# Performance work log

Measured on AMD Instinct MI355X. Metric: run time of the kernel, lower is better.

The kernel has to match this reference:

```python
import jax, jax.numpy as jnp
import numpy as np

B, T, V, E, H = 32, 128, 32000, 512, 1024
START = 1


def setup_inputs() -> dict:
    key = jax.random.key(0)
    ks = jax.random.split(key, 16)
    s = 0.02
    inp = {
        'h0': jax.random.normal(ks[0], (B, H), jnp.float32),
        'c0': jax.random.normal(ks[1], (B, H), jnp.float32),
        'h1': jax.random.normal(ks[2], (B, H), jnp.float32),
        'c1': jax.random.normal(ks[3], (B, H), jnp.float32),
        'h2': jax.random.normal(ks[4], (B, H), jnp.float32),
        'c2': jax.random.normal(ks[5], (B, H), jnp.float32),
        'h3': jax.random.normal(ks[6], (B, H), jnp.float32),
        'c3': jax.random.normal(ks[7], (B, H), jnp.float32),
        'emb': jax.random.normal(ks[8], (V, E), jnp.float32) * s,
        'Wx0': jax.random.normal(ks[9], (E, 4 * H), jnp.float32) * s,
        'Wh0': jax.random.normal(ks[10], (H, 4 * H), jnp.float32) * s,
        'b0': jnp.zeros((4 * H,), jnp.float32),
        'Wx1': jax.random.normal(ks[11], (H, 4 * H), jnp.float32) * s,
        'Wh1': jax.random.normal(ks[12], (H, 4 * H), jnp.float32) * s,
        'b1': jnp.zeros((4 * H,), jnp.float32),
        'Wx2': jax.random.normal(ks[13], (H, 4 * H), jnp.float32) * s,
        'Wh2': jax.random.normal(ks[14], (H, 4 * H), jnp.float32) * s,
        'b2': jnp.zeros((4 * H,), jnp.float32),
        'Wx3': jax.random.normal(ks[15], (H, 4 * H), jnp.float32) * s,
        'Wh3': jax.random.normal(jax.random.fold_in(key, 99), (H, 4 * H), jnp.float32) * s,
        'b3': jnp.zeros((4 * H,), jnp.float32),
        'fcW': jax.random.normal(jax.random.fold_in(key, 100), (H, V), jnp.float32) * s,
        'fcb': jnp.zeros((V,), jnp.float32),
        'target_length': T,
    }
    return inp


def _lstm_cell(x, h, c, Wx, Wh, b):
    # Keras gate order: i, f, c(candidate), o
    z = x @ Wx + h @ Wh + b  # [B, 4H]
    i, f, g, o = jnp.split(z, 4, axis=-1)
    i = jax.nn.sigmoid(i)
    f = jax.nn.sigmoid(f)
    g = jnp.tanh(g)
    o = jax.nn.sigmoid(o)
    c_new = f * c + i * g
    h_new = o * jnp.tanh(c_new)
    return h_new, c_new


def reference(h0, c0, h1, c1, h2, c2, h3, c3, emb,
              Wx0, Wh0, b0, Wx1, Wh1, b1, Wx2, Wh2, b2, Wx3, Wh3, b3,
              fcW, fcb, target_length):
    n_batch = h0.shape[0]
    tok0 = jnp.full((n_batch,), START, dtype=jnp.int32)

    def step(carry, _):
        tok, h0, c0, h1, c1, h2, c2, h3, c3 = carry
        x = emb[tok]  # [B, E]
        h0, c0 = _lstm_cell(x, h0, c0, Wx0, Wh0, b0)
        h1, c1 = _lstm_cell(h0, h1, c1, Wx1, Wh1, b1)
        h2, c2 = _lstm_cell(h1, h2, c2, Wx2, Wh2, b2)
        h3, c3 = _lstm_cell(h2, h3, c3, Wx3, Wh3, b3)
        logits = h3 @ fcW + fcb  # [B, V]
        tok = jnp.argmax(logits, axis=1).astype(jnp.int32)
        return (tok, h0, c0, h1, c1, h2, c2, h3, c3), (logits, tok)

    carry0 = (tok0, h0, c0, h1, c1, h2, c2, h3, c3)
    _, (logits_seq, ids_seq) = jax.lax.scan(step, carry0, None, length=target_length)
    outputs_prob = jnp.transpose(logits_seq, (1, 0, 2))  # [B, T, V]
    outputs = jnp.transpose(ids_seq, (1, 0))             # [B, T]
    return outputs_prob, outputs
```

## Files before the change

kernel.cpp:

```cpp
#include <hip/hip_runtime.h>
#include <stdint.h>

#define NBLK 256
#define NTHR 512

typedef _Float16 f16;
typedef _Float16 f16x8 __attribute__((ext_vector_type(8)));
typedef float f32x4 __attribute__((ext_vector_type(4)));
typedef unsigned long long u64;


__device__ __forceinline__ void split2(float w, f16& hi, f16& lo) {
  f16 h = (__builtin_fabsf(w) < 6.104e-05f) ? (f16)0.0f : (f16)w;
  hi = h;
  lo = (f16)((w - (float)h) * 2048.0f);
}

__device__ __forceinline__ void split3(float w, f16& h, f16& l, f16& m) {
  const float hf = (__builtin_fabsf(w) < 6.104e-05f) ? 0.0f : (float)(f16)w;
  h = (f16)hf;
  const float r1s = (w - hf) * 2048.0f;
  const float lf = (__builtin_fabsf(r1s) < 6.104e-05f) ? 0.0f : (float)(f16)r1s;
  l = (f16)lf;
  const float r2s = (r1s - lf) * 2048.0f;
  m = (__builtin_fabsf(r2s) < 6.104e-05f) ? (f16)0.0f : (f16)r2s;
}

__device__ __forceinline__ float sig32(float z) {
  const float e32 = (float)exp(-(double)z);
  return 1.0f / __fadd_rn(1.0f, e32);
}
__device__ __forceinline__ float tanh32f(float z) { return (float)tanh((double)z); }

__device__ __forceinline__ u64 packvc(float v, unsigned col) {
  unsigned u = __float_as_uint(v);
  u = (u & 0x80000000u) ? ~u : (u | 0x80000000u);
  return ((u64)u << 32) | (u64)(0xFFFFFFFFu - col);
}
__device__ __forceinline__ u64 umax64(u64 a, u64 b) { return a > b ? a : b; }


struct MainP {
  const float* emb;
  const float* bias[4];
  const float* fcb;
  const float* hini[4];
  const float* cini[4];
  const f16* Whi[4];
  const f16* Wlo[4];
  const f16* fchi;
  const f16* fclo;
  f16* axh[5];
  f16* axl[5];
  f16* axm[5];
  u64* top;
  unsigned* bar;
  float* out;
};

struct PrepP {
  const float* src[9];
  f16* dhi[9];
  f16* dlo[9];
  int srcK[9];
  int srcN[9];
  int dstK[9];
  int koff[9];
  int base[9];
  unsigned* bar;
};


__device__ __forceinline__ void grid_barrier(unsigned* cnt, unsigned* gen) {
  __syncthreads();
  if (threadIdx.x == 0) {
    unsigned g = __hip_atomic_load(gen, __ATOMIC_RELAXED, __HIP_MEMORY_SCOPE_AGENT);
    unsigned prev = __hip_atomic_fetch_add(cnt, 1u, __ATOMIC_ACQ_REL, __HIP_MEMORY_SCOPE_AGENT);
    if (prev == (unsigned)(NBLK - 1)) {
      __hip_atomic_store(cnt, 0u, __ATOMIC_RELAXED, __HIP_MEMORY_SCOPE_AGENT);
      __hip_atomic_store(gen, g + 1u, __ATOMIC_RELEASE, __HIP_MEMORY_SCOPE_AGENT);
    } else {
      while (__hip_atomic_load(gen, __ATOMIC_RELAXED, __HIP_MEMORY_SCOPE_AGENT) == g) {
        __builtin_amdgcn_s_sleep(1);
      }
      __builtin_amdgcn_fence(__ATOMIC_ACQUIRE, "agent");
    }
  }
  __syncthreads();
}


__global__ __launch_bounds__(256) void prep_split(PrepP p) {
  const int bid = blockIdx.x;
  const int tid = threadIdx.x;
  if (bid == 0 && tid == 0) { p.bar[0] = 0; p.bar[1] = 0; }

  int job = 0;
#pragma unroll
  for (int j2 = 1; j2 < 9; ++j2) job += (bid >= p.base[j2]) ? 1 : 0;
  const int tile = bid - p.base[job];
  const float* src = p.src[job];
  f16* dhi = p.dhi[job];
  f16* dlo = p.dlo[job];
  const int srcN = p.srcN[job];
  const int dstK = p.dstK[job];
  const int koff = p.koff[job];
  const int nK = p.srcK[job] >> 6;
  const int tk = tile % nK;
  const int tc = tile / nK;

  __shared__ float lds[64][65];
  {
    const int j = tid & 63, i0 = tid >> 6;
#pragma unroll
    for (int r = 0; r < 16; ++r) {
      const int i = r * 4 + i0;
      lds[i][j] = src[(size_t)(tk * 64 + i) * srcN + tc * 64 + j];
    }
  }
  __syncthreads();
  {
    const int jc = tid >> 2, part = tid & 3;
    f16x8 h0v, l0v, h1v, l1v;
#pragma unroll
    for (int ii = 0; ii < 8; ++ii) {
      f16 a, b;
      split2(lds[part * 16 + ii][jc], a, b);
      h0v[ii] = a; l0v[ii] = b;
    }
#pragma unroll
    for (int ii = 0; ii < 8; ++ii) {
      f16 a, b;
      split2(lds[part * 16 + 8 + ii][jc], a, b);
      h1v[ii] = a; l1v[ii] = b;
    }
    const size_t db = (size_t)(tc * 64 + jc) * dstK + koff + tk * 64 + part * 16;
    *(f16x8*)(dhi + db) = h0v;
    *(f16x8*)(dhi + db + 8) = h1v;
    *(f16x8*)(dlo + db) = l0v;
    *(f16x8*)(dlo + db + 8) = l1v;
  }
}

__global__ void ws_sentinel(float* out) {
  if (blockIdx.x == 0 && threadIdx.x == 0) out[0] = 1.0e9f;
}


__global__ __launch_bounds__(NTHR, 2) void lstm_main(MainP p) {
  const int blk = blockIdx.x;
  const int tid = threadIdx.x;
  const int lane = tid & 63;
  const int w = tid >> 6;
  const int q = lane >> 4;
  const int n16 = lane & 15;

  __shared__ float zpart[8][2][32][16];
  __shared__ float fcpart[2][32][128];
  __shared__ float zred[32][16];
  __shared__ float cst[4][32][4];
  __shared__ f16 hs_h[32][4];
  __shared__ f16 hs_l[32][4];
  __shared__ f16 hs_m[32][4];
  __shared__ int tokS[32];
  __shared__ u64 redu[32][16];

  unsigned* bcnt = p.bar;
  unsigned* bgen = p.bar + 1;

  for (int i = tid; i < 512; i += NTHR) {
    const int l = i >> 7, b = (i >> 2) & 31, j = i & 3;
    cst[l][b][j] = p.cini[l][b * 1024 + 4 * blk + j];
    f16 hh, ll, mm;
    split3(p.hini[l][b * 1024 + 4 * blk + j], hh, ll, mm);
    if (l == 0) {
      p.axh[0][b * 1024 + 4 * blk + j] = hh;
      p.axl[0][b * 1024 + 4 * blk + j] = ll;
      p.axm[0][b * 1024 + 4 * blk + j] = mm;
    } else {
      p.axh[l][b * 2048 + 1024 + 4 * blk + j] = hh;
      p.axl[l][b * 2048 + 1024 + 4 * blk + j] = ll;
      p.axm[l][b * 2048 + 1024 + 4 * blk + j] = mm;
    }
  }
  grid_barrier(bcnt, bgen);

  const int col16 = 1024 * (n16 >> 2) + 4 * blk + (n16 & 3);

  auto layer_tail = [&](int l, const float* bias, f16* dh, f16* dl, f16* dm, int dstride) {
    __syncthreads();
    {
      const int row = tid >> 4, c = tid & 15;
      double A = 0.0, B = 0.0;
#pragma unroll
      for (int w2 = 0; w2 < 8; ++w2) {
        A += (double)zpart[w2][0][row][c];
        B += (double)zpart[w2][1][row][c];
      }
      zred[row][c] = __fadd_rn(__fadd_rn((float)A, (float)B),
                               bias[1024 * (c >> 2) + 4 * blk + (c & 3)]);
    }
    __syncthreads();
    if (tid < 128) {
      const int b = tid >> 2, j = tid & 3;
      const float zi = zred[b][j], zf = zred[b][4 + j], zg = zred[b][8 + j], zo = zred[b][12 + j];
      const float i_ = sig32(zi);
      const float f_ = sig32(zf);
      const float g_ = tanh32f(zg);
      const float o_ = sig32(zo);
      const float c_ = __fadd_rn(__fmul_rn(f_, cst[l][b][j]), __fmul_rn(i_, g_));
      cst[l][b][j] = c_;
      const float h_ = __fmul_rn(o_, tanh32f(c_));
      f16 hh, ll, mm;
      split3(h_, hh, ll, mm);
      hs_h[b][j] = hh; hs_l[b][j] = ll; hs_m[b][j] = mm;
      dh[b * dstride + 4 * blk + j] = hh;
      dl[b * dstride + 4 * blk + j] = ll;
      dm[b * dstride + 4 * blk + j] = mm;
    }
  };

  for (int t = 0; t < 128; ++t) {
    if (t == 0) {
      if (tid < 32) tokS[tid] = 1;
    } else {
      const int row = tid >> 4, seg = tid & 15;
      const u64* tr = p.top + row * 256 + seg * 16;
      u64 m = 0;
#pragma unroll
      for (int e = 0; e < 16; ++e) m = umax64(m, tr[e]);
      redu[row][seg] = m;
      __syncthreads();
      if (tid < 32) {
        u64 mm = redu[tid][0];
#pragma unroll
        for (int s2 = 1; s2 < 16; ++s2) mm = umax64(mm, redu[tid][s2]);
        const int tok = (int)(0xFFFFFFFFu - (unsigned)(mm & 0xFFFFFFFFull));
        tokS[tid] = tok;
        if (blk == tid)
          p.out[(size_t)32 * 128 * 32000 + (size_t)tid * 128 + (t - 1)] = (float)tok;
      }
    }
    __syncthreads();

    {
      double zdA0[4] = {0,0,0,0}, zdA1[4] = {0,0,0,0};
      double zdB0[4] = {0,0,0,0}, zdB1[4] = {0,0,0,0};
      const size_t wrow = (size_t)col16 * 1536;
      const f32x4 zz = {0.f, 0.f, 0.f, 0.f};
#pragma unroll
      for (int sl = 0; sl < 6; ++sl) {
        const int k0 = (w * 6 + sl) * 32 + 8 * q;
        const f16x8 bh = *(const f16x8*)(p.Whi[0] + wrow + k0);
        const f16x8 bl = *(const f16x8*)(p.Wlo[0] + wrow + k0);
        f16x8 ah0, al0, am0, ah1, al1, am1;
        if (k0 < 512) {
          {
            const float* ep = p.emb + (size_t)tokS[n16] * 512 + k0;
            const float4 v0 = *(const float4*)ep;
            const float4 v1 = *(const float4*)(ep + 4);
            const float vv[8] = {v0.x, v0.y, v0.z, v0.w, v1.x, v1.y, v1.z, v1.w};
#pragma unroll
            for (int e = 0; e < 8; ++e) { f16 a,b,c; split3(vv[e],a,b,c); ah0[e]=a; al0[e]=b; am0[e]=c; }
          }
          {
            const float* ep = p.emb + (size_t)tokS[16 + n16] * 512 + k0;
            const float4 v0 = *(const float4*)ep;
            const float4 v1 = *(const float4*)(ep + 4);
            const float vv[8] = {v0.x, v0.y, v0.z, v0.w, v1.x, v1.y, v1.z, v1.w};
#pragma unroll
            for (int e = 0; e < 8; ++e) { f16 a,b,c; split3(vv[e],a,b,c); ah1[e]=a; al1[e]=b; am1[e]=c; }
          }
        } else {
          const int ks = k0 - 512;
          ah0 = *(const f16x8*)(p.axh[0] + n16 * 1024 + ks);
          al0 = *(const f16x8*)(p.axl[0] + n16 * 1024 + ks);
          am0 = *(const f16x8*)(p.axm[0] + n16 * 1024 + ks);
          ah1 = *(const f16x8*)(p.axh[0] + (16 + n16) * 1024 + ks);
          al1 = *(const f16x8*)(p.axl[0] + (16 + n16) * 1024 + ks);
          am1 = *(const f16x8*)(p.axm[0] + (16 + n16) * 1024 + ks);
        }
        f32x4 t00 = __builtin_amdgcn_mfma_f32_16x16x32_f16(ah0, bh, zz, 0, 0, 0);
        f32x4 t10 = __builtin_amdgcn_mfma_f32_16x16x32_f16(ah0, bl, zz, 0, 0, 0);
        t10 = __builtin_amdgcn_mfma_f32_16x16x32_f16(al0, bh, t10, 0, 0, 0);
        f32x4 t20 = __builtin_amdgcn_mfma_f32_16x16x32_f16(al0, bl, zz, 0, 0, 0);
        t20 = __builtin_amdgcn_mfma_f32_16x16x32_f16(am0, bh, t20, 0, 0, 0);
        f32x4 t01 = __builtin_amdgcn_mfma_f32_16x16x32_f16(ah1, bh, zz, 0, 0, 0);
        f32x4 t11 = __builtin_amdgcn_mfma_f32_16x16x32_f16(ah1, bl, zz, 0, 0, 0);
        t11 = __builtin_amdgcn_mfma_f32_16x16x32_f16(al1, bh, t11, 0, 0, 0);
        f32x4 t21 = __builtin_amdgcn_mfma_f32_16x16x32_f16(al1, bl, zz, 0, 0, 0);
        t21 = __builtin_amdgcn_mfma_f32_16x16x32_f16(am1, bh, t21, 0, 0, 0);
        if (k0 < 512) {
#pragma unroll
          for (int r = 0; r < 4; ++r) {
            zdA0[r] += (double)t00[r] + (double)t10[r] * 0x1p-11 + (double)t20[r] * 0x1p-22;
            zdA1[r] += (double)t01[r] + (double)t11[r] * 0x1p-11 + (double)t21[r] * 0x1p-22;
          }
        } else {
#pragma unroll
          for (int r = 0; r < 4; ++r) {
            zdB0[r] += (double)t00[r] + (double)t10[r] * 0x1p-11 + (double)t20[r] * 0x1p-22;
            zdB1[r] += (double)t01[r] + (double)t11[r] * 0x1p-11 + (double)t21[r] * 0x1p-22;
          }
        }
      }
#pragma unroll
      for (int r = 0; r < 4; ++r) {
        zpart[w][0][4 * q + r][n16] = (float)zdA0[r];
        zpart[w][0][16 + 4 * q + r][n16] = (float)zdA1[r];
        zpart[w][1][4 * q + r][n16] = (float)zdB0[r];
        zpart[w][1][16 + 4 * q + r][n16] = (float)zdB1[r];
      }
    }
    layer_tail(0, p.bias[0], p.axh[1], p.axl[1], p.axm[1], 2048);
    grid_barrier(bcnt, bgen);

    for (int l = 1; l < 4; ++l) {
      if (tid < 128) {
        const int b = tid >> 2, j = tid & 3;
        if (l == 1) {
          p.axh[0][b * 1024 + 4 * blk + j] = hs_h[b][j];
          p.axl[0][b * 1024 + 4 * blk + j] = hs_l[b][j];
          p.axm[0][b * 1024 + 4 * blk + j] = hs_m[b][j];
        } else {
          p.axh[l - 1][b * 2048 + 1024 + 4 * blk + j] = hs_h[b][j];
          p.axl[l - 1][b * 2048 + 1024 + 4 * blk + j] = hs_l[b][j];
          p.axm[l - 1][b * 2048 + 1024 + 4 * blk + j] = hs_m[b][j];
        }
      }
      {
        double zdA0[4] = {0,0,0,0}, zdA1[4] = {0,0,0,0};
        double zdB0[4] = {0,0,0,0}, zdB1[4] = {0,0,0,0};
        const f16* Whi_ = p.Whi[l];
        const f16* Wlo_ = p.Wlo[l];
        const f16* axh_ = p.axh[l];
        const f16* axl_ = p.axl[l];
        const f16* axm_ = p.axm[l];
        const size_t wrow = (size_t)col16 * 2048;
        const f32x4 zz = {0.f, 0.f, 0.f, 0.f};
#pragma unroll
        for (int sl = 0; sl < 8; ++sl) {
          const int k0 = (w * 8 + sl) * 32 + 8 * q;
          const f16x8 bh = *(const f16x8*)(Whi_ + wrow + k0);
          const f16x8 bl = *(const f16x8*)(Wlo_ + wrow + k0);
          const f16x8 ah0 = *(const f16x8*)(axh_ + n16 * 2048 + k0);
          const f16x8 al0 = *(const f16x8*)(axl_ + n16 * 2048 + k0);
          const f16x8 am0 = *(const f16x8*)(axm_ + n16 * 2048 + k0);
          const f16x8 ah1 = *(const f16x8*)(axh_ + (16 + n16) * 2048 + k0);
          const f16x8 al1 = *(const f16x8*)(axl_ + (16 + n16) * 2048 + k0);
          const f16x8 am1 = *(const f16x8*)(axm_ + (16 + n16) * 2048 + k0);
          f32x4 t00 = __builtin_amdgcn_mfma_f32_16x16x32_f16(ah0, bh, zz, 0, 0, 0);
          f32x4 t10 = __builtin_amdgcn_mfma_f32_16x16x32_f16(ah0, bl, zz, 0, 0, 0);
          t10 = __builtin_amdgcn_mfma_f32_16x16x32_f16(al0, bh, t10, 0, 0, 0);
          f32x4 t20 = __builtin_amdgcn_mfma_f32_16x16x32_f16(al0, bl, zz, 0, 0, 0);
          t20 = __builtin_amdgcn_mfma_f32_16x16x32_f16(am0, bh, t20, 0, 0, 0);
          f32x4 t01 = __builtin_amdgcn_mfma_f32_16x16x32_f16(ah1, bh, zz, 0, 0, 0);
          f32x4 t11 = __builtin_amdgcn_mfma_f32_16x16x32_f16(ah1, bl, zz, 0, 0, 0);
          t11 = __builtin_amdgcn_mfma_f32_16x16x32_f16(al1, bh, t11, 0, 0, 0);
          f32x4 t21 = __builtin_amdgcn_mfma_f32_16x16x32_f16(al1, bl, zz, 0, 0, 0);
          t21 = __builtin_amdgcn_mfma_f32_16x16x32_f16(am1, bh, t21, 0, 0, 0);
          if (k0 < 1024) {
#pragma unroll
            for (int r = 0; r < 4; ++r) {
              zdA0[r] += (double)t00[r] + (double)t10[r] * 0x1p-11 + (double)t20[r] * 0x1p-22;
              zdA1[r] += (double)t01[r] + (double)t11[r] * 0x1p-11 + (double)t21[r] * 0x1p-22;
            }
          } else {
#pragma unroll
            for (int r = 0; r < 4; ++r) {
              zdB0[r] += (double)t00[r] + (double)t10[r] * 0x1p-11 + (double)t20[r] * 0x1p-22;
              zdB1[r] += (double)t01[r] + (double)t11[r] * 0x1p-11 + (double)t21[r] * 0x1p-22;
            }
          }
        }
#pragma unroll
        for (int r = 0; r < 4; ++r) {
          zpart[w][0][4 * q + r][n16] = (float)zdA0[r];
          zpart[w][0][16 + 4 * q + r][n16] = (float)zdA1[r];
          zpart[w][1][4 * q + r][n16] = (float)zdB0[r];
          zpart[w][1][16 + 4 * q + r][n16] = (float)zdB1[r];
        }
      }
      if (l < 3) layer_tail(l, p.bias[l], p.axh[l + 1], p.axl[l + 1], p.axm[l + 1], 2048);
      else       layer_tail(l, p.bias[l], p.axh[4], p.axl[4], p.axm[4], 1024);
      grid_barrier(bcnt, bgen);
    }

    if (tid < 128) {
      const int b = tid >> 2, j = tid & 3;
      p.axh[3][b * 2048 + 1024 + 4 * blk + j] = hs_h[b][j];
      p.axl[3][b * 2048 + 1024 + 4 * blk + j] = hs_l[b][j];
      p.axm[3][b * 2048 + 1024 + 4 * blk + j] = hs_m[b][j];
    }
    {
      const int kh = w & 1;
      const int tg = w >> 1;
      double LdA0[4] = {0,0,0,0}, LdA1[4] = {0,0,0,0};
      double LdB0[4] = {0,0,0,0}, LdB1[4] = {0,0,0,0};
      const int clA = (tg * 2 + 0) * 16 + n16;
      const int clB = (tg * 2 + 1) * 16 + n16;
      const size_t fbA = (size_t)(125 * blk + (clA < 125 ? clA : 124)) * 1024;
      const size_t fbB = (size_t)(125 * blk + (clB < 125 ? clB : 124)) * 1024;
      const f32x4 zz = {0.f, 0.f, 0.f, 0.f};
#pragma unroll
      for (int sl = 0; sl < 16; ++sl) {
        const int k0 = (kh * 16 + sl) * 32 + 8 * q;
        const f16x8 ah0 = *(const f16x8*)(p.axh[4] + n16 * 1024 + k0);
        const f16x8 al0 = *(const f16x8*)(p.axl[4] + n16 * 1024 + k0);
        const f16x8 am0 = *(const f16x8*)(p.axm[4] + n16 * 1024 + k0);
        const f16x8 ah1 = *(const f16x8*)(p.axh[4] + (16 + n16) * 1024 + k0);
        const f16x8 al1 = *(const f16x8*)(p.axl[4] + (16 + n16) * 1024 + k0);
        const f16x8 am1 = *(const f16x8*)(p.axm[4] + (16 + n16) * 1024 + k0);
        {
          const f16x8 bh = *(const f16x8*)(p.fchi + fbA + k0);
          const f16x8 bl = *(const f16x8*)(p.fclo + fbA + k0);
          f32x4 t00 = __builtin_amdgcn_mfma_f32_16x16x32_f16(ah0, bh, zz, 0, 0, 0);
          f32x4 t10 = __builtin_amdgcn_mfma_f32_16x16x32_f16(ah0, bl, zz, 0, 0, 0);
          t10 = __builtin_amdgcn_mfma_f32_16x16x32_f16(al0, bh, t10, 0, 0, 0);
          f32x4 t20 = __builtin_amdgcn_mfma_f32_16x16x32_f16(al0, bl, zz, 0, 0, 0);
          t20 = __builtin_amdgcn_mfma_f32_16x16x32_f16(am0, bh, t20, 0, 0, 0);
          f32x4 t01 = __builtin_amdgcn_mfma_f32_16x16x32_f16(ah1, bh, zz, 0, 0, 0);
          f32x4 t11 = __builtin_amdgcn_mfma_f32_16x16x32_f16(ah1, bl, zz, 0, 0, 0);
          t11 = __builtin_amdgcn_mfma_f32_16x16x32_f16(al1, bh, t11, 0, 0, 0);
          f32x4 t21 = __builtin_amdgcn_mfma_f32_16x16x32_f16(al1, bl, zz, 0, 0, 0);
          t21 = __builtin_amdgcn_mfma_f32_16x16x32_f16(am1, bh, t21, 0, 0, 0);
#pragma unroll
          for (int r = 0; r < 4; ++r) {
            LdA0[r] += (double)t00[r] + (double)t10[r] * 0x1p-11 + (double)t20[r] * 0x1p-22;
            LdA1[r] += (double)t01[r] + (double)t11[r] * 0x1p-11 + (double)t21[r] * 0x1p-22;
          }
        }
        {
          const f16x8 bh = *(const f16x8*)(p.fchi + fbB + k0);
          const f16x8 bl = *(const f16x8*)(p.fclo + fbB + k0);
          f32x4 t00 = __builtin_amdgcn_mfma_f32_16x16x32_f16(ah0, bh, zz, 0, 0, 0);
          f32x4 t10 = __builtin_amdgcn_mfma_f32_16x16x32_f16(ah0, bl, zz, 0, 0, 0);
          t10 = __builtin_amdgcn_mfma_f32_16x16x32_f16(al0, bh, t10, 0, 0, 0);
          f32x4 t20 = __builtin_amdgcn_mfma_f32_16x16x32_f16(al0, bl, zz, 0, 0, 0);
          t20 = __builtin_amdgcn_mfma_f32_16x16x32_f16(am0, bh, t20, 0, 0, 0);
          f32x4 t01 = __builtin_amdgcn_mfma_f32_16x16x32_f16(ah1, bh, zz, 0, 0, 0);
          f32x4 t11 = __builtin_amdgcn_mfma_f32_16x16x32_f16(ah1, bl, zz, 0, 0, 0);
          t11 = __builtin_amdgcn_mfma_f32_16x16x32_f16(al1, bh, t11, 0, 0, 0);
          f32x4 t21 = __builtin_amdgcn_mfma_f32_16x16x32_f16(al1, bl, zz, 0, 0, 0);
          t21 = __builtin_amdgcn_mfma_f32_16x16x32_f16(am1, bh, t21, 0, 0, 0);
#pragma unroll
          for (int r = 0; r < 4; ++r) {
            LdB0[r] += (double)t00[r] + (double)t10[r] * 0x1p-11 + (double)t20[r] * 0x1p-22;
            LdB1[r] += (double)t01[r] + (double)t11[r] * 0x1p-11 + (double)t21[r] * 0x1p-22;
          }
        }
      }
#pragma unroll
      for (int r = 0; r < 4; ++r) {
        fcpart[kh][4 * q + r][(tg * 2 + 0) * 16 + n16] = (float)LdA0[r];
        fcpart[kh][16 + 4 * q + r][(tg * 2 + 0) * 16 + n16] = (float)LdA1[r];
        fcpart[kh][4 * q + r][(tg * 2 + 1) * 16 + n16] = (float)LdB0[r];
        fcpart[kh][16 + 4 * q + r][(tg * 2 + 1) * 16 + n16] = (float)LdB1[r];
      }
    }
    __syncthreads();
    {
      const int row = tid >> 4, cg = tid & 15;
      u64 best = 0;
      float* orow = p.out + (size_t)row * (128 * 32000) + (size_t)t * 32000 + 125 * blk;
      const float* fb = p.fcb + 125 * blk;
#pragma unroll
      for (int cc = 0; cc < 8; ++cc) {
        const int c = cg * 8 + cc;
        if (c < 125) {
          const float z32 = (float)((double)fcpart[0][row][c] + (double)fcpart[1][row][c]);
          const float z = __fadd_rn(z32, fb[c]);
          __builtin_nontemporal_store(z, orow + c);
          best = umax64(best, packvc(z, (unsigned)(125 * blk + c)));
        }
      }
      redu[row][cg] = best;
    }
    __syncthreads();
    if (tid < 32) {
      u64 mm = redu[tid][0];
#pragma unroll
      for (int s2 = 1; s2 < 16; ++s2) mm = umax64(mm, redu[tid][s2]);
      p.top[tid * 256 + blk] = mm;
    }
    grid_barrier(bcnt, bgen);
  }

  if (blk < 32) {
    if (tid < 16) {
      const u64* tr = p.top + blk * 256 + tid * 16;
      u64 m = 0;
#pragma unroll
      for (int e = 0; e < 16; ++e) m = umax64(m, tr[e]);
      redu[0][tid] = m;
    }
    __syncthreads();
    if (tid == 0) {
      u64 mm = redu[0][0];
#pragma unroll
      for (int s2 = 1; s2 < 16; ++s2) mm = umax64(mm, redu[0][s2]);
      p.out[(size_t)32 * 128 * 32000 + (size_t)blk * 128 + 127] =
          (float)(0xFFFFFFFFu - (unsigned)(mm & 0xFFFFFFFFull));
    }
  }
}


extern "C" void kernel_launch(void* const* d_in, const int* in_sizes, int n_in,
                              void* d_out, int out_size, void* d_ws, size_t ws_size,
                              hipStream_t stream) {
  (void)in_sizes; (void)n_in; (void)out_size;
  const float* hini[4] = {(const float*)d_in[0], (const float*)d_in[2], (const float*)d_in[4], (const float*)d_in[6]};
  const float* cini[4] = {(const float*)d_in[1], (const float*)d_in[3], (const float*)d_in[5], (const float*)d_in[7]};
  const float* emb = (const float*)d_in[8];
  const float* Wx[4] = {(const float*)d_in[9], (const float*)d_in[12], (const float*)d_in[15], (const float*)d_in[18]};
  const float* Wh[4] = {(const float*)d_in[10], (const float*)d_in[13], (const float*)d_in[16], (const float*)d_in[19]};
  const float* bias[4] = {(const float*)d_in[11], (const float*)d_in[14], (const float*)d_in[17], (const float*)d_in[20]};
  const float* fcW = (const float*)d_in[21];
  const float* fcb = (const float*)d_in[22];

  char* ws = (char*)d_ws;
  size_t off = 0;
  auto take = [&](size_t bytes) -> char* {
    char* r = ws + off;
    off += (bytes + 255) & ~(size_t)255;
    return r;
  };
  f16* Whi[4]; f16* Wlo[4];
  Whi[0] = (f16*)take((size_t)4096 * 1536 * 2);
  Wlo[0] = (f16*)take((size_t)4096 * 1536 * 2);
  for (int l = 1; l < 4; ++l) {
    Whi[l] = (f16*)take((size_t)4096 * 2048 * 2);
    Wlo[l] = (f16*)take((size_t)4096 * 2048 * 2);
  }
  f16* fchi = (f16*)take((size_t)32000 * 1024 * 2);
  f16* fclo = (f16*)take((size_t)32000 * 1024 * 2);
  f16* axh[5]; f16* axl[5]; f16* axm[5];
  const int axsz[5] = {1024, 2048, 2048, 2048, 1024};
  for (int l = 0; l < 5; ++l) {
    axh[l] = (f16*)take((size_t)32 * axsz[l] * 2);
    axl[l] = (f16*)take((size_t)32 * axsz[l] * 2);
    axm[l] = (f16*)take((size_t)32 * axsz[l] * 2);
  }
  u64* top = (u64*)take((size_t)32 * 256 * 8);
  unsigned* bar = (unsigned*)take(256);

  if (off > ws_size) {
    hipLaunchKernelGGL(ws_sentinel, dim3(1), dim3(1), 0, stream, (float*)d_out);
    return;
  }

  PrepP pp;
  pp.src[0] = Wx[0]; pp.src[1] = Wh[0]; pp.src[2] = Wx[1]; pp.src[3] = Wh[1];
  pp.src[4] = Wx[2]; pp.src[5] = Wh[2]; pp.src[6] = Wx[3]; pp.src[7] = Wh[3];
  pp.src[8] = fcW;
  const int dj[8] = {0, 0, 1, 1, 2, 2, 3, 3};
  for (int j = 0; j < 8; ++j) { pp.dhi[j] = Whi[dj[j]]; pp.dlo[j] = Wlo[dj[j]]; }
  pp.dhi[8] = fchi; pp.dlo[8] = fclo;
  const int srcK[9] = {512, 1024, 1024, 1024, 1024, 1024, 1024, 1024, 1024};
  const int srcN[9] = {4096, 4096, 4096, 4096, 4096, 4096, 4096, 4096, 32000};
  const int dstK[9] = {1536, 1536, 2048, 2048, 2048, 2048, 2048, 2048, 1024};
  const int koff[9] = {0, 512, 0, 1024, 0, 1024, 0, 1024, 0};
  const int base[9] = {0, 512, 1536, 2560, 3584, 4608, 5632, 6656, 7680};
  for (int j = 0; j < 9; ++j) {
    pp.srcK[j] = srcK[j]; pp.srcN[j] = srcN[j]; pp.dstK[j] = dstK[j];
    pp.koff[j] = koff[j]; pp.base[j] = base[j];
  }
  pp.bar = bar;
  hipLaunchKernelGGL(prep_split, dim3(15680), dim3(256), 0, stream, pp);

  MainP mp;
  mp.emb = emb;
  for (int l = 0; l < 4; ++l) {
    mp.bias[l] = bias[l]; mp.hini[l] = hini[l]; mp.cini[l] = cini[l];
    mp.Whi[l] = Whi[l]; mp.Wlo[l] = Wlo[l];
  }
  mp.fcb = fcb; mp.fchi = fchi; mp.fclo = fclo;
  for (int l = 0; l < 5; ++l) { mp.axh[l] = axh[l]; mp.axl[l] = axl[l]; mp.axm[l] = axm[l]; }
  mp.top = top; mp.bar = bar; mp.out = (float*)d_out;

  void* args[] = {&mp};
  hipLaunchCooperativeKernel((void*)lstm_main, dim3(NBLK), dim3(NTHR), args, 0, stream);
}
```

Baseline: 34.39 ms.

## Pre-swizzle weights into MFMA fragment order and double threads per block

```diff
diff --git a/kernel.cpp b/kernel.cpp
--- a/kernel.cpp
+++ b/kernel.cpp
@@ -2,7 +2,7 @@
 #include <stdint.h>
 
 #define NBLK 256
-#define NTHR 512
+#define NTHR 1024
 
 typedef _Float16 f16;
 typedef _Float16 f16x8 __attribute__((ext_vector_type(8)));
@@ -39,6 +39,11 @@
 }
 __device__ __forceinline__ u64 umax64(u64 a, u64 b) { return a > b ? a : b; }
 
+__device__ __forceinline__ size_t faddr(int k, int row) {
+  return (size_t)(((k >> 5) * 2 + (row >> 4)) * 512 +
+                  (16 * ((k >> 3) & 3) + (row & 15)) * 8 + (k & 7));
+}
+
 
 struct MainP {
   const float* emb;
@@ -46,28 +51,16 @@
   const float* fcb;
   const float* hini[4];
   const float* cini[4];
-  const f16* Whi[4];
-  const f16* Wlo[4];
-  const f16* fchi;
-  const f16* fclo;
+  const f16* WfH[4];
+  const f16* WfL[4];
+  const f16* fcH;
+  const f16* fcL;
   f16* axh[5];
   f16* axl[5];
   f16* axm[5];
   u64* top;
   unsigned* bar;
   float* out;
-};
-
-struct PrepP {
-  const float* src[9];
-  f16* dhi[9];
-  f16* dlo[9];
-  int srcK[9];
-  int srcN[9];
-  int dstK[9];
-  int koff[9];
-  int base[9];
-  unsigned* bar;
 };
 
 
@@ -90,56 +83,57 @@
 }
 
 
-__global__ __launch_bounds__(256) void prep_split(PrepP p) {
-  const int bid = blockIdx.x;
-  const int tid = threadIdx.x;
-  if (bid == 0 && tid == 0) { p.bar[0] = 0; p.bar[1] = 0; }
-
-  int job = 0;
-#pragma unroll
-  for (int j2 = 1; j2 < 9; ++j2) job += (bid >= p.base[j2]) ? 1 : 0;
-  const int tile = bid - p.base[job];
-  const float* src = p.src[job];
-  f16* dhi = p.dhi[job];
-  f16* dlo = p.dlo[job];
-  const int srcN = p.srcN[job];
-  const int dstK = p.dstK[job];
-  const int koff = p.koff[job];
-  const int nK = p.srcK[job] >> 6;
-  const int tk = tile % nK;
-  const int tc = tile / nK;
-
-  __shared__ float lds[64][65];
-  {
-    const int j = tid & 63, i0 = tid >> 6;
-#pragma unroll
-    for (int r = 0; r < 16; ++r) {
-      const int i = r * 4 + i0;
-      lds[i][j] = src[(size_t)(tk * 64 + i) * srcN + tc * 64 + j];
-    }
-  }
-  __syncthreads();
-  {
-    const int jc = tid >> 2, part = tid & 3;
-    f16x8 h0v, l0v, h1v, l1v;
-#pragma unroll
-    for (int ii = 0; ii < 8; ++ii) {
-      f16 a, b;
-      split2(lds[part * 16 + ii][jc], a, b);
-      h0v[ii] = a; l0v[ii] = b;
-    }
-#pragma unroll
-    for (int ii = 0; ii < 8; ++ii) {
-      f16 a, b;
-      split2(lds[part * 16 + 8 + ii][jc], a, b);
-      h1v[ii] = a; l1v[ii] = b;
-    }
-    const size_t db = (size_t)(tc * 64 + jc) * dstK + koff + tk * 64 + part * 16;
-    *(f16x8*)(dhi + db) = h0v;
-    *(f16x8*)(dhi + db + 8) = h1v;
-    *(f16x8*)(dlo + db) = l0v;
-    *(f16x8*)(dlo + db + 8) = l1v;
-  }
+__global__ __launch_bounds__(256) void prep_lstm(const float* Wx, const float* Wh,
+                                                 int Kx, int CH, f16* dh, f16* dl) {
+  const int id = blockIdx.x * 256 + threadIdx.x;
+  const int lane = id & 63;
+  const int cw = id >> 6;
+  const int tile = cw / CH;
+  if (tile >= 256) return;
+  const int chunk = cw - tile * CH;
+  const int n16 = lane & 15, qq = lane >> 4;
+  const int col = 1024 * (n16 >> 2) + 4 * tile + (n16 & 3);
+  const int kb = chunk * 32 + 8 * qq;
+  f16x8 hv, lv;
+#pragma unroll
+  for (int e = 0; e < 8; ++e) {
+    const int k = kb + e;
+    const float wv = (k < Kx) ? Wx[(size_t)k * 4096 + col] : Wh[(size_t)(k - Kx) * 4096 + col];
+    f16 h, l;
+    split2(wv, h, l);
+    hv[e] = h; lv[e] = l;
+  }
+  const size_t d = ((size_t)cw * 64 + lane) * 8;
+  *(f16x8*)(dh + d) = hv;
+  *(f16x8*)(dl + d) = lv;
+}
+
+__global__ __launch_bounds__(256) void prep_fc(const float* fcW, f16* dh, f16* dl,
+                                               unsigned* bar) {
+  const int id = blockIdx.x * 256 + threadIdx.x;
+  if (id == 0) { bar[0] = 0; bar[1] = 0; }
+  const int lane = id & 63;
+  const int cw = id >> 6;
+  const int chunk = cw & 31;
+  const int stb = cw >> 5;
+  const int st = stb & 7, blk = stb >> 3;
+  if (blk >= 256) return;
+  const int n16 = lane & 15, qq = lane >> 4;
+  int cl = st * 16 + n16;
+  if (cl > 124) cl = 124;
+  const int col = 125 * blk + cl;
+  const int kb = chunk * 32 + 8 * qq;
+  f16x8 hv, lv;
+#pragma unroll
+  for (int e = 0; e < 8; ++e) {
+    const float wv = fcW[(size_t)(kb + e) * 32000 + col];
+    f16 h, l;
+    split2(wv, h, l);
+    hv[e] = h; lv[e] = l;
+  }
+  const size_t d = ((size_t)cw * 64 + lane) * 8;
+  *(f16x8*)(dh + d) = hv;
+  *(f16x8*)(dl + d) = lv;
 }
 
 __global__ void ws_sentinel(float* out) {
@@ -147,7 +141,7 @@
 }
 
 
-__global__ __launch_bounds__(NTHR, 2) void lstm_main(MainP p) {
+__global__ __launch_bounds__(NTHR, 4) void lstm_main(MainP p) {
   const int blk = blockIdx.x;
   const int tid = threadIdx.x;
   const int lane = tid & 63;
@@ -155,13 +149,11 @@
   const int q = lane >> 4;
   const int n16 = lane & 15;
 
-  __shared__ float zpart[8][2][32][16];
+  __shared__ float zpart[16][2][32][16];
   __shared__ float fcpart[2][32][128];
   __shared__ float zred[32][16];
   __shared__ float cst[4][32][4];
-  __shared__ f16 hs_h[32][4];
-  __shared__ f16 hs_l[32][4];
-  __shared__ f16 hs_m[32][4];
+  __shared__ f16 hs_h[32][4], hs_l[32][4], hs_m[32][4];
   __shared__ int tokS[32];
   __shared__ u64 redu[32][16];
 
@@ -173,27 +165,21 @@
     cst[l][b][j] = p.cini[l][b * 1024 + 4 * blk + j];
     f16 hh, ll, mm;
     split3(p.hini[l][b * 1024 + 4 * blk + j], hh, ll, mm);
-    if (l == 0) {
-      p.axh[0][b * 1024 + 4 * blk + j] = hh;
-      p.axl[0][b * 1024 + 4 * blk + j] = ll;
-      p.axm[0][b * 1024 + 4 * blk + j] = mm;
-    } else {
-      p.axh[l][b * 2048 + 1024 + 4 * blk + j] = hh;
-      p.axl[l][b * 2048 + 1024 + 4 * blk + j] = ll;
-      p.axm[l][b * 2048 + 1024 + 4 * blk + j] = mm;
-    }
+    const int kp = (l == 0) ? (4 * blk + j) : (1024 + 4 * blk + j);
+    const size_t a = faddr(kp, b);
+    p.axh[l][a] = hh;
+    p.axl[l][a] = ll;
+    p.axm[l][a] = mm;
   }
   grid_barrier(bcnt, bgen);
 
-  const int col16 = 1024 * (n16 >> 2) + 4 * blk + (n16 & 3);
-
-  auto layer_tail = [&](int l, const float* bias, f16* dh, f16* dl, f16* dm, int dstride) {
+  auto layer_tail = [&](int l, const float* bias, f16* dh, f16* dl, f16* dm) {
     __syncthreads();
-    {
+    if (tid < 512) {
       const int row = tid >> 4, c = tid & 15;
       double A = 0.0, B = 0.0;
 #pragma unroll
-      for (int w2 = 0; w2 < 8; ++w2) {
+      for (int w2 = 0; w2 < 16; ++w2) {
         A += (double)zpart[w2][0][row][c];
         B += (double)zpart[w2][1][row][c];
       }
@@ -214,9 +200,8 @@
       f16 hh, ll, mm;
       split3(h_, hh, ll, mm);
       hs_h[b][j] = hh; hs_l[b][j] = ll; hs_m[b][j] = mm;
-      dh[b * dstride + 4 * blk + j] = hh;
-      dl[b * dstride + 4 * blk + j] = ll;
-      dm[b * dstride + 4 * blk + j] = mm;
+      const size_t a = faddr(4 * blk + j, b);
+      dh[a] = hh; dl[a] = ll; dm[a] = mm;
     }
   };
 
@@ -224,12 +209,14 @@
     if (t == 0) {
       if (tid < 32) tokS[tid] = 1;
     } else {
-      const int row = tid >> 4, seg = tid & 15;
-      const u64* tr = p.top + row * 256 + seg * 16;
-      u64 m = 0;
-#pragma unroll
-      for (int e = 0; e < 16; ++e) m = umax64(m, tr[e]);
-      redu[row][seg] = m;
+      if (tid < 512) {
+        const int row = tid >> 4, seg = tid & 15;
+        const u64* tr = p.top + row * 256 + seg * 16;
+        u64 m = 0;
+#pragma unroll
+        for (int e = 0; e < 16; ++e) m = umax64(m, tr[e]);
+        redu[row][seg] = m;
+      }
       __syncthreads();
       if (tid < 32) {
         u64 mm = redu[tid][0];
@@ -246,15 +233,17 @@
     {
       double zdA0[4] = {0,0,0,0}, zdA1[4] = {0,0,0,0};
       double zdB0[4] = {0,0,0,0}, zdB1[4] = {0,0,0,0};
-      const size_t wrow = (size_t)col16 * 1536;
       const f32x4 zz = {0.f, 0.f, 0.f, 0.f};
 #pragma unroll
-      for (int sl = 0; sl < 6; ++sl) {
-        const int k0 = (w * 6 + sl) * 32 + 8 * q;
-        const f16x8 bh = *(const f16x8*)(p.Whi[0] + wrow + k0);
-        const f16x8 bl = *(const f16x8*)(p.Wlo[0] + wrow + k0);
+      for (int sl = 0; sl < 3; ++sl) {
+        const int chunk = w * 3 + sl;
+        const int k0 = chunk * 32 + 8 * q;
+        const f16x8 bh = __builtin_nontemporal_load(
+            (const f16x8*)(p.WfH[0] + ((size_t)(blk * 48 + chunk) * 64 + lane) * 8));
+        const f16x8 bl = __builtin_nontemporal_load(
+            (const f16x8*)(p.WfL[0] + ((size_t)(blk * 48 + chunk) * 64 + lane) * 8));
         f16x8 ah0, al0, am0, ah1, al1, am1;
-        if (k0 < 512) {
+        if (chunk < 16) {
           {
             const float* ep = p.emb + (size_t)tokS[n16] * 512 + k0;
             const float4 v0 = *(const float4*)ep;
@@ -272,13 +261,14 @@
             for (int e = 0; e < 8; ++e) { f16 a,b,c; split3(vv[e],a,b,c); ah1[e]=a; al1[e]=b; am1[e]=c; }
           }
         } else {
-          const int ks = k0 - 512;
-          ah0 = *(const f16x8*)(p.axh[0] + n16 * 1024 + ks);
-          al0 = *(const f16x8*)(p.axl[0] + n16 * 1024 + ks);
-          am0 = *(const f16x8*)(p.axm[0] + n16 * 1024 + ks);
-          ah1 = *(const f16x8*)(p.axh[0] + (16 + n16) * 1024 + ks);
-          al1 = *(const f16x8*)(p.axl[0] + (16 + n16) * 1024 + ks);
-          am1 = *(const f16x8*)(p.axm[0] + (16 + n16) * 1024 + ks);
+          const int cs = chunk - 16;
+          const size_t b0 = (size_t)(cs * 2) * 512 + lane * 8;
+          ah0 = *(const f16x8*)(p.axh[0] + b0);
+          al0 = *(const f16x8*)(p.axl[0] + b0);
+          am0 = *(const f16x8*)(p.axm[0] + b0);
+          ah1 = *(const f16x8*)(p.axh[0] + b0 + 512);
+          al1 = *(const f16x8*)(p.axl[0] + b0 + 512);
+          am1 = *(const f16x8*)(p.axm[0] + b0 + 512);
         }
         f32x4 t00 = __builtin_amdgcn_mfma_f32_16x16x32_f16(ah0, bh, zz, 0, 0, 0);
         f32x4 t10 = __builtin_amdgcn_mfma_f32_16x16x32_f16(ah0, bl, zz, 0, 0, 0);
@@ -290,7 +280,7 @@
         t11 = __builtin_amdgcn_mfma_f32_16x16x32_f16(al1, bh, t11, 0, 0, 0);
         f32x4 t21 = __builtin_amdgcn_mfma_f32_16x16x32_f16(al1, bl, zz, 0, 0, 0);
         t21 = __builtin_amdgcn_mfma_f32_16x16x32_f16(am1, bh, t21, 0, 0, 0);
-        if (k0 < 512) {
+        if (chunk < 16) {
 #pragma unroll
           for (int r = 0; r < 4; ++r) {
             zdA0[r] += (double)t00[r] + (double)t10[r] * 0x1p-11 + (double)t20[r] * 0x1p-22;
@@ -312,43 +302,41 @@
         zpart[w][1][16 + 4 * q + r][n16] = (float)zdB1[r];
       }
     }
-    layer_tail(0, p.bias[0], p.axh[1], p.axl[1], p.axm[1], 2048);
+    layer_tail(0, p.bias[0], p.axh[1], p.axl[1], p.axm[1]);
     grid_barrier(bcnt, bgen);
 
     for (int l = 1; l < 4; ++l) {
       if (tid < 128) {
         const int b = tid >> 2, j = tid & 3;
-        if (l == 1) {
-          p.axh[0][b * 1024 + 4 * blk + j] = hs_h[b][j];
-          p.axl[0][b * 1024 + 4 * blk + j] = hs_l[b][j];
-          p.axm[0][b * 1024 + 4 * blk + j] = hs_m[b][j];
-        } else {
-          p.axh[l - 1][b * 2048 + 1024 + 4 * blk + j] = hs_h[b][j];
-          p.axl[l - 1][b * 2048 + 1024 + 4 * blk + j] = hs_l[b][j];
-          p.axm[l - 1][b * 2048 + 1024 + 4 * blk + j] = hs_m[b][j];
-        }
+        const int kp = (l == 1) ? (4 * blk + j) : (1024 + 4 * blk + j);
+        const size_t a = faddr(kp, b);
+        p.axh[l - 1][a] = hs_h[b][j];
+        p.axl[l - 1][a] = hs_l[b][j];
+        p.axm[l - 1][a] = hs_m[b][j];
       }
       {
         double zdA0[4] = {0,0,0,0}, zdA1[4] = {0,0,0,0};
         double zdB0[4] = {0,0,0,0}, zdB1[4] = {0,0,0,0};
-        const f16* Whi_ = p.Whi[l];
-        const f16* Wlo_ = p.Wlo[l];
+        const f16* WH = p.WfH[l];
+        const f16* WL = p.WfL[l];
         const f16* axh_ = p.axh[l];
         const f16* axl_ = p.axl[l];
         const f16* axm_ = p.axm[l];
-        const size_t wrow = (size_t)col16 * 2048;
         const f32x4 zz = {0.f, 0.f, 0.f, 0.f};
 #pragma unroll
-        for (int sl = 0; sl < 8; ++sl) {
-          const int k0 = (w * 8 + sl) * 32 + 8 * q;
-          const f16x8 bh = *(const f16x8*)(Whi_ + wrow + k0);
-          const f16x8 bl = *(const f16x8*)(Wlo_ + wrow + k0);
-          const f16x8 ah0 = *(const f16x8*)(axh_ + n16 * 2048 + k0);
-          const f16x8 al0 = *(const f16x8*)(axl_ + n16 * 2048 + k0);
-          const f16x8 am0 = *(const f16x8*)(axm_ + n16 * 2048 + k0);
-          const f16x8 ah1 = *(const f16x8*)(axh_ + (16 + n16) * 2048 + k0);
-          const f16x8 al1 = *(const f16x8*)(axl_ + (16 + n16) * 2048 + k0);
-          const f16x8 am1 = *(const f16x8*)(axm_ + (16 + n16) * 2048 + k0);
+        for (int sl = 0; sl < 4; ++sl) {
+          const int chunk = w * 4 + sl;
+          const f16x8 bh = __builtin_nontemporal_load(
+              (const f16x8*)(WH + ((size_t)(blk * 64 + chunk) * 64 + lane) * 8));
+          const f16x8 bl = __builtin_nontemporal_load(
+              (const f16x8*)(WL + ((size_t)(blk * 64 + chunk) * 64 + lane) * 8));
+          const size_t b0 = (size_t)(chunk * 2) * 512 + lane * 8;
+          const f16x8 ah0 = *(const f16x8*)(axh_ + b0);
+          const f16x8 al0 = *(const f16x8*)(axl_ + b0);
+          const f16x8 am0 = *(const f16x8*)(axm_ + b0);
+          const f16x8 ah1 = *(const f16x8*)(axh_ + b0 + 512);
+          const f16x8 al1 = *(const f16x8*)(axl_ + b0 + 512);
+          const f16x8 am1 = *(const f16x8*)(axm_ + b0 + 512);
           f32x4 t00 = __builtin_amdgcn_mfma_f32_16x16x32_f16(ah0, bh, zz, 0, 0, 0);
           f32x4 t10 = __builtin_amdgcn_mfma_f32_16x16x32_f16(ah0, bl, zz, 0, 0, 0);
           t10 = __builtin_amdgcn_mfma_f32_16x16x32_f16(al0, bh, t10, 0, 0, 0);
@@ -359,7 +347,7 @@
           t11 = __builtin_amdgcn_mfma_f32_16x16x32_f16(al1, bh, t11, 0, 0, 0);
           f32x4 t21 = __builtin_amdgcn_mfma_f32_16x16x32_f16(al1, bl, zz, 0, 0, 0);
           t21 = __builtin_amdgcn_mfma_f32_16x16x32_f16(am1, bh, t21, 0, 0, 0);
-          if (k0 < 1024) {
+          if (chunk < 32) {
 #pragma unroll
             for (int r = 0; r < 4; ++r) {
               zdA0[r] += (double)t00[r] + (double)t10[r] * 0x1p-11 + (double)t20[r] * 0x1p-22;
@@ -381,85 +369,60 @@
           zpart[w][1][16 + 4 * q + r][n16] = (float)zdB1[r];
         }
       }
-      if (l < 3) layer_tail(l, p.bias[l], p.axh[l + 1], p.axl[l + 1], p.axm[l + 1], 2048);
-      else       layer_tail(l, p.bias[l], p.axh[4], p.axl[4], p.axm[4], 1024);
+      if (l < 3) layer_tail(l, p.bias[l], p.axh[l + 1], p.axl[l + 1], p.axm[l + 1]);
+      else       layer_tail(l, p.bias[l], p.axh[4], p.axl[4], p.axm[4]);
       grid_barrier(bcnt, bgen);
     }
 
     if (tid < 128) {
       const int b = tid >> 2, j = tid & 3;
-      p.axh[3][b * 2048 + 1024 + 4 * blk + j] = hs_h[b][j];
-      p.axl[3][b * 2048 + 1024 + 4 * blk + j] = hs_l[b][j];
-      p.axm[3][b * 2048 + 1024 + 4 * blk + j] = hs_m[b][j];
+      const size_t a = faddr(1024 + 4 * blk + j, b);
+      p.axh[3][a] = hs_h[b][j];
+      p.axl[3][a] = hs_l[b][j];
+      p.axm[3][a] = hs_m[b][j];
     }
     {
       const int kh = w & 1;
-      const int tg = w >> 1;
-      double LdA0[4] = {0,0,0,0}, LdA1[4] = {0,0,0,0};
-      double LdB0[4] = {0,0,0,0}, LdB1[4] = {0,0,0,0};
-      const int clA = (tg * 2 + 0) * 16 + n16;
-      const int clB = (tg * 2 + 1) * 16 + n16;
-      const size_t fbA = (size_t)(125 * blk + (clA < 125 ? clA : 124)) * 1024;
-      const size_t fbB = (size_t)(125 * blk + (clB < 125 ? clB : 124)) * 1024;
+      const int st = w >> 1;
+      double Ld0[4] = {0,0,0,0}, Ld1[4] = {0,0,0,0};
       const f32x4 zz = {0.f, 0.f, 0.f, 0.f};
 #pragma unroll
       for (int sl = 0; sl < 16; ++sl) {
-        const int k0 = (kh * 16 + sl) * 32 + 8 * q;
-        const f16x8 ah0 = *(const f16x8*)(p.axh[4] + n16 * 1024 + k0);
-        const f16x8 al0 = *(const f16x8*)(p.axl[4] + n16 * 1024 + k0);
-        const f16x8 am0 = *(const f16x8*)(p.axm[4] + n16 * 1024 + k0);
-        const f16x8 ah1 = *(const f16x8*)(p.axh[4] + (16 + n16) * 1024 + k0);
-        const f16x8 al1 = *(const f16x8*)(p.axl[4] + (16 + n16) * 1024 + k0);
-        const f16x8 am1 = *(const f16x8*)(p.axm[4] + (16 + n16) * 1024 + k0);
-        {
-          const f16x8 bh = *(const f16x8*)(p.fchi + fbA + k0);
-          const f16x8 bl = *(const f16x8*)(p.fclo + fbA + k0);
-          f32x4 t00 = __builtin_amdgcn_mfma_f32_16x16x32_f16(ah0, bh, zz, 0, 0, 0);
-          f32x4 t10 = __builtin_amdgcn_mfma_f32_16x16x32_f16(ah0, bl, zz, 0, 0, 0);
-          t10 = __builtin_amdgcn_mfma_f32_16x16x32_f16(al0, bh, t10, 0, 0, 0);
-          f32x4 t20 = __builtin_amdgcn_mfma_f32_16x16x32_f16(al0, bl, zz, 0, 0, 0);
-          t20 = __builtin_amdgcn_mfma_f32_16x16x32_f16(am0, bh, t20, 0, 0, 0);
-          f32x4 t01 = __builtin_amdgcn_mfma_f32_16x16x32_f16(ah1, bh, zz, 0, 0, 0);
-          f32x4 t11 = __builtin_amdgcn_mfma_f32_16x16x32_f16(ah1, bl, zz, 0, 0, 0);
-          t11 = __builtin_amdgcn_mfma_f32_16x16x32_f16(al1, bh, t11, 0, 0, 0);
-          f32x4 t21 = __builtin_amdgcn_mfma_f32_16x16x32_f16(al1, bl, zz, 0, 0, 0);
-          t21 = __builtin_amdgcn_mfma_f32_16x16x32_f16(am1, bh, t21, 0, 0, 0);
-#pragma unroll
-          for (int r = 0; r < 4; ++r) {
-            LdA0[r] += (double)t00[r] + (double)t10[r] * 0x1p-11 + (double)t20[r] * 0x1p-22;
-            LdA1[r] += (double)t01[r] + (double)t11[r] * 0x1p-11 + (double)t21[r] * 0x1p-22;
-          }
+        const int chunk = kh * 16 + sl;
+        const size_t ab = (size_t)(chunk * 2) * 512 + lane * 8;
+        const f16x8 ah0 = *(const f16x8*)(p.axh[4] + ab);
+        const f16x8 al0 = *(const f16x8*)(p.axl[4] + ab);
+        const f16x8 am0 = *(const f16x8*)(p.axm[4] + ab);
+        const f16x8 ah1 = *(const f16x8*)(p.axh[4] + ab + 512);
+        const f16x8 al1 = *(const f16x8*)(p.axl[4] + ab + 512);
+        const f16x8 am1 = *(const f16x8*)(p.axm[4] + ab + 512);
+        const size_t wb = (((size_t)(blk * 8 + st) * 32 + chunk) * 64 + lane) * 8;
+        const f16x8 bh = *(const f16x8*)(p.fcH + wb);
+        const f16x8 bl = *(const f16x8*)(p.fcL + wb);
+        f32x4 t00 = __builtin_amdgcn_mfma_f32_16x16x32_f16(ah0, bh, zz, 0, 0, 0);
+        f32x4 t10 = __builtin_amdgcn_mfma_f32_16x16x32_f16(ah0, bl, zz, 0, 0, 0);
+        t10 = __builtin_amdgcn_mfma_f32_16x16x32_f16(al0, bh, t10, 0, 0, 0);
+        f32x4 t20 = __builtin_amdgcn_mfma_f32_16x16x32_f16(al0, bl, zz, 0, 0, 0);
+        t20 = __builtin_amdgcn_mfma_f32_16x16x32_f16(am0, bh, t20, 0, 0, 0);
+        f32x4 t01 = __builtin_amdgcn_mfma_f32_16x16x32_f16(ah1, bh, zz, 0, 0, 0);
+        f32x4 t11 = __builtin_amdgcn_mfma_f32_16x16x32_f16(ah1, bl, zz, 0, 0, 0);
+        t11 = __builtin_amdgcn_mfma_f32_16x16x32_f16(al1, bh, t11, 0, 0, 0);
+        f32x4 t21 = __builtin_amdgcn_mfma_f32_16x16x32_f16(al1, bl, zz, 0, 0, 0);
+        t21 = __builtin_amdgcn_mfma_f32_16x16x32_f16(am1, bh, t21, 0, 0, 0);
+#pragma unroll
+        for (int r = 0; r < 4; ++r) {
+          Ld0[r] += (double)t00[r] + (double)t10[r] * 0x1p-11 + (double)t20[r] * 0x1p-22;
+          Ld1[r] += (double)t01[r] + (double)t11[r] * 0x1p-11 + (double)t21[r] * 0x1p-22;
         }
-        {
-          const f16x8 bh = *(const f16x8*)(p.fchi + fbB + k0);
-          const f16x8 bl = *(const f16x8*)(p.fclo + fbB + k0);
-          f32x4 t00 = __builtin_amdgcn_mfma_f32_16x16x32_f16(ah0, bh, zz, 0, 0, 0);
-          f32x4 t10 = __builtin_amdgcn_mfma_f32_16x16x32_f16(ah0, bl, zz, 0, 0, 0);
-          t10 = __builtin_amdgcn_mfma_f32_16x16x32_f16(al0, bh, t10, 0, 0, 0);
-          f32x4 t20 = __builtin_amdgcn_mfma_f32_16x16x32_f16(al0, bl, zz, 0, 0, 0);
-          t20 = __builtin_amdgcn_mfma_f32_16x16x32_f16(am0, bh, t20, 0, 0, 0);
-          f32x4 t01 = __builtin_amdgcn_mfma_f32_16x16x32_f16(ah1, bh, zz, 0, 0, 0);
-          f32x4 t11 = __builtin_amdgcn_mfma_f32_16x16x32_f16(ah1, bl, zz, 0, 0, 0);
-          t11 = __builtin_amdgcn_mfma_f32_16x16x32_f16(al1, bh, t11, 0, 0, 0);
-          f32x4 t21 = __builtin_amdgcn_mfma_f32_16x16x32_f16(al1, bl, zz, 0, 0, 0);
-          t21 = __builtin_amdgcn_mfma_f32_16x16x32_f16(am1, bh, t21, 0, 0, 0);
-#pragma unroll
-          for (int r = 0; r < 4; ++r) {
-            LdB0[r] += (double)t00[r] + (double)t10[r] * 0x1p-11 + (double)t20[r] * 0x1p-22;
-            LdB1[r] += (double)t01[r] + (double)t11[r] * 0x1p-11 + (double)t21[r] * 0x1p-22;
-          }
-        }
       }
 #pragma unroll
       for (int r = 0; r < 4; ++r) {
-        fcpart[kh][4 * q + r][(tg * 2 + 0) * 16 + n16] = (float)LdA0[r];
-        fcpart[kh][16 + 4 * q + r][(tg * 2 + 0) * 16 + n16] = (float)LdA1[r];
-        fcpart[kh][4 * q + r][(tg * 2 + 1) * 16 + n16] = (float)LdB0[r];
-        fcpart[kh][16 + 4 * q + r][(tg * 2 + 1) * 16 + n16] = (float)LdB1[r];
+        fcpart[kh][4 * q + r][st * 16 + n16] = (float)Ld0[r];
+        fcpart[kh][16 + 4 * q + r][st * 16 + n16] = (float)Ld1[r];
       }
     }
     __syncthreads();
-    {
+    if (tid < 512) {
       const int row = tid >> 4, cg = tid & 15;
       u64 best = 0;
       float* orow = p.out + (size_t)row * (128 * 32000) + (size_t)t * 32000 + 125 * blk;
@@ -526,21 +489,21 @@
     off += (bytes + 255) & ~(size_t)255;
     return r;
   };
-  f16* Whi[4]; f16* Wlo[4];
-  Whi[0] = (f16*)take((size_t)4096 * 1536 * 2);
-  Wlo[0] = (f16*)take((size_t)4096 * 1536 * 2);
+  f16* WfH[4]; f16* WfL[4];
+  WfH[0] = (f16*)take((size_t)256 * 48 * 64 * 8 * 2);
+  WfL[0] = (f16*)take((size_t)256 * 48 * 64 * 8 * 2);
   for (int l = 1; l < 4; ++l) {
-    Whi[l] = (f16*)take((size_t)4096 * 2048 * 2);
-    Wlo[l] = (f16*)take((size_t)4096 * 2048 * 2);
-  }
-  f16* fchi = (f16*)take((size_t)32000 * 1024 * 2);
-  f16* fclo = (f16*)take((size_t)32000 * 1024 * 2);
+    WfH[l] = (f16*)take((size_t)256 * 64 * 64 * 8 * 2);
+    WfL[l] = (f16*)take((size_t)256 * 64 * 64 * 8 * 2);
+  }
+  f16* fcH = (f16*)take((size_t)256 * 8 * 32 * 64 * 8 * 2);
+  f16* fcL = (f16*)take((size_t)256 * 8 * 32 * 64 * 8 * 2);
   f16* axh[5]; f16* axl[5]; f16* axm[5];
-  const int axsz[5] = {1024, 2048, 2048, 2048, 1024};
+  const int axK[5] = {1024, 2048, 2048, 2048, 1024};
   for (int l = 0; l < 5; ++l) {
-    axh[l] = (f16*)take((size_t)32 * axsz[l] * 2);
-    axl[l] = (f16*)take((size_t)32 * axsz[l] * 2);
-    axm[l] = (f16*)take((size_t)32 * axsz[l] * 2);
+    axh[l] = (f16*)take((size_t)axK[l] * 32 * 2);
+    axl[l] = (f16*)take((size_t)axK[l] * 32 * 2);
+    axm[l] = (f16*)take((size_t)axK[l] * 32 * 2);
   }
   u64* top = (u64*)take((size_t)32 * 256 * 8);
   unsigned* bar = (unsigned*)take(256);
@@ -550,32 +513,21 @@
     return;
   }
 
-  PrepP pp;
-  pp.src[0] = Wx[0]; pp.src[1] = Wh[0]; pp.src[2] = Wx[1]; pp.src[3] = Wh[1];
-  pp.src[4] = Wx[2]; pp.src[5] = Wh[2]; pp.src[6] = Wx[3]; pp.src[7] = Wh[3];
-  pp.src[8] = fcW;
-  const int dj[8] = {0, 0, 1, 1, 2, 2, 3, 3};
-  for (int j = 0; j < 8; ++j) { pp.dhi[j] = Whi[dj[j]]; pp.dlo[j] = Wlo[dj[j]]; }
-  pp.dhi[8] = fchi; pp.dlo[8] = fclo;
-  const int srcK[9] = {512, 1024, 1024, 1024, 1024, 1024, 1024, 1024, 1024};
-  const int srcN[9] = {4096, 4096, 4096, 4096, 4096, 4096, 4096, 4096, 32000};
-  const int dstK[9] = {1536, 1536, 2048, 2048, 2048, 2048, 2048, 2048, 1024};
-  const int koff[9] = {0, 512, 0, 1024, 0, 1024, 0, 1024, 0};
-  const int base[9] = {0, 512, 1536, 2560, 3584, 4608, 5632, 6656, 7680};
-  for (int j = 0; j < 9; ++j) {
-    pp.srcK[j] = srcK[j]; pp.srcN[j] = srcN[j]; pp.dstK[j] = dstK[j];
-    pp.koff[j] = koff[j]; pp.base[j] = base[j];
-  }
-  pp.bar = bar;
-  hipLaunchKernelGGL(prep_split, dim3(15680), dim3(256), 0, stream, pp);
+  hipLaunchKernelGGL(prep_lstm, dim3(256 * 48 * 64 / 256), dim3(256), 0, stream,
+                     Wx[0], Wh[0], 512, 48, WfH[0], WfL[0]);
+  for (int l = 1; l < 4; ++l)
+    hipLaunchKernelGGL(prep_lstm, dim3(256 * 64 * 64 / 256), dim3(256), 0, stream,
+                       Wx[l], Wh[l], 1024, 64, WfH[l], WfL[l]);
+  hipLaunchKernelGGL(prep_fc, dim3(256 * 8 * 32 * 64 / 256), dim3(256), 0, stream,
+                     fcW, fcH, fcL, bar);
 
   MainP mp;
   mp.emb = emb;
   for (int l = 0; l < 4; ++l) {
     mp.bias[l] = bias[l]; mp.hini[l] = hini[l]; mp.cini[l] = cini[l];
-    mp.Whi[l] = Whi[l]; mp.Wlo[l] = Wlo[l];
-  }
-  mp.fcb = fcb; mp.fchi = fchi; mp.fclo = fclo;
+    mp.WfH[l] = WfH[l]; mp.WfL[l] = WfL[l];
+  }
+  mp.fcb = fcb; mp.fcH = fcH; mp.fcL = fcL;
   for (int l = 0; l < 5; ++l) { mp.axh[l] = axh[l]; mp.axl[l] = axl[l]; mp.axm[l] = axm[l]; }
   mp.top = top; mp.bar = bar; mp.out = (float*)d_out;
 
```

New measurement: 34.55 ms. Within noise of the previous version (+0.4%).
